# Optimization experiments

Hardware: AMD Instinct MI355X
Metric: run time of the kernel (lower is better)

## Reference

```python
import jax, jax.numpy as jnp
import numpy as np

B, S, D = 2, 2048, 512
H = 8
G = 4
LAMBDA_INIT = 0.2  # 0.8 - 0.6*exp(-0.3*(layer_idx-1)) with layer_idx=1
EPS = 1e-5


def setup_inputs() -> dict:
    key = jax.random.key(0)
    ks = jax.random.split(key, 16)
    n = jax.random.normal
    return {
        "x": n(ks[0], (B, S, D), jnp.float32),
        "K1_w": n(ks[1], (D, D), jnp.float32) * 0.02,
        "K1_b": n(ks[2], (D,), jnp.float32) * 0.02,
        "Q1_w": n(ks[3], (D, D), jnp.float32) * 0.02,
        "K2_w": n(ks[4], (D, D), jnp.float32) * 0.02,
        "K2_b": n(ks[5], (D,), jnp.float32) * 0.02,
        "Q2_w": n(ks[6], (D, D), jnp.float32) * 0.02,
        "V_w": n(ks[7], (D, D), jnp.float32) * 0.02,
        "lambda_q1": n(ks[8], (H, 1), jnp.float32),
        "lambda_k1": n(ks[9], (H, 1), jnp.float32),
        "lambda_q2": n(ks[10], (H, 1), jnp.float32),
        "lambda_k2": n(ks[11], (H, 1), jnp.float32),
        "gn_w": jnp.ones((D,), jnp.float32),
        "gn_b": jnp.zeros((D,), jnp.float32),
        "out_w": n(ks[12], (D, D), jnp.float32) * 0.02,
        "out_b": n(ks[13], (D,), jnp.float32) * 0.02,
    }


def reference(x, K1_w, K1_b, Q1_w, K2_w, K2_b, Q2_w, V_w,
              lambda_q1, lambda_k1, lambda_q2, lambda_k2,
              gn_w, gn_b, out_w, out_b):
    b, s, d = x.shape
    hd = d // H

    def heads(t):  # (b,s,d) -> (b,H,s,hd)
        return t.reshape(b, s, H, hd).transpose(0, 2, 1, 3)

    q1 = heads(x @ Q1_w.T)
    k1 = heads(x @ K1_w.T + K1_b)
    q2 = heads(x @ Q2_w.T)
    k2 = heads(x @ K2_w.T + K2_b)
    v = heads(x @ V_w.T)

    scale = hd ** 0.5
    a1 = jax.nn.softmax(jnp.einsum('bhqd,bhkd->bhqk', q1, k1) / scale, axis=-1)
    a2 = jax.nn.softmax(jnp.einsum('bhqd,bhkd->bhqk', q2, k2) / scale, axis=-1)

    lam = (jnp.exp(lambda_q1 * lambda_k1)
           - jnp.exp(lambda_q2 * lambda_k2) + LAMBDA_INIT)  # (H,1)
    attn = a1 - lam.reshape(1, H, 1, 1) * a2

    o = jnp.einsum('bhqk,bhkd->bhqd', attn, v)
    o = o.transpose(0, 2, 1, 3).reshape(b, s, d)

    # GroupNorm over channels: input (b, d, s), groups G normalize over (d/G, s)
    xc = o.transpose(0, 2, 1).reshape(b, G, d // G, s)
    mu = xc.mean(axis=(2, 3), keepdims=True)
    var = xc.var(axis=(2, 3), keepdims=True)
    xn = ((xc - mu) * jax.lax.rsqrt(var + EPS)).reshape(b, d, s)
    xn = xn * gn_w[None, :, None] + gn_b[None, :, None]

    y = xn.transpose(0, 2, 1) @ out_w.T + out_b
    return y
```

## Files before the change

### kernel.cpp

```cpp
#include <hip/hip_runtime.h>
#include <hip/hip_bf16.h>

typedef __bf16 bf16;
typedef __attribute__((ext_vector_type(4))) __bf16 bf16x4;
typedef __attribute__((ext_vector_type(8))) __bf16 bf16x8;
typedef __attribute__((ext_vector_type(4))) float f32x4;

#define MFMA16(a, b, c) __builtin_amdgcn_mfma_f32_16x16x32_bf16((a), (b), (c), 0, 0, 0)

static constexpr float EPS = 1e-5f;
static constexpr float LAMBDA_INIT = 0.2f;
static constexpr float LOG2E = 1.44269504088896340736f;

__device__ __forceinline__ bf16x8 cvt8(const float* p) {
    const f32x4 a = *(const f32x4*)p;
    const f32x4 b = *(const f32x4*)(p + 4);
    bf16x8 r;
    r[0] = (bf16)a[0]; r[1] = (bf16)a[1]; r[2] = (bf16)a[2]; r[3] = (bf16)a[3];
    r[4] = (bf16)b[0]; r[5] = (bf16)b[1]; r[6] = (bf16)b[2]; r[7] = (bf16)b[3];
    return r;
}

__device__ __forceinline__ void gload_lds16(const void* g, void* l) {
    __builtin_amdgcn_global_load_lds(
        (const __attribute__((address_space(1))) unsigned int*)g,
        (__attribute__((address_space(3))) unsigned int*)l,
        16, 0, 0);
}

__global__ __launch_bounds__(256) void prep_kernel(
    const float* __restrict__ x,
    const float* __restrict__ q1w, const float* __restrict__ k1w,
    const float* __restrict__ q2w, const float* __restrict__ k2w,
    const float* __restrict__ vw,
    const float* __restrict__ ow, const float* __restrict__ gnw,
    const float* __restrict__ gnb,
    bf16* __restrict__ xb, bf16* __restrict__ wb,
    bf16* __restrict__ owg, float* __restrict__ S0, float* __restrict__ stats)
{
    const int tid = threadIdx.x;
    if (blockIdx.x < 1664) {
        const size_t base = ((size_t)blockIdx.x * 256 + tid) * 8;
        if (base < 2097152) {
            *(bf16x8*)(xb + base) = cvt8(x + base);
        } else {
            const size_t wbase = base - 2097152;
            const int wsel = (int)(wbase >> 18);
            const size_t off = wbase & 262143;
            const float* W = (wsel == 0) ? q1w : (wsel == 1) ? k1w :
                             (wsel == 2) ? q2w : (wsel == 3) ? k2w : vw;
            *(bf16x8*)(wb + wbase) = cvt8(W + off);
        }
        return;
    }

    __shared__ float red[4];
    const int pb = blockIdx.x - 1664;
    if (pb == 0 && tid < 16) stats[tid] = 0.f;

    const int n0 = pb * 16;
    const int c0 = tid, c1 = tid + 256;
    const float gw0 = gnw[c0], gw1 = gnw[c1];
    const float gb0 = gnb[c0], gb1 = gnb[c1];

    for (int n = 0; n < 16; ++n) {
        const size_t rowb = (size_t)(n0 + n) * 512;
        const float w0 = ow[rowb + c0];
        const float w1 = ow[rowb + c1];
        owg[rowb + c0] = (bf16)(w0 * gw0);
        owg[rowb + c1] = (bf16)(w1 * gw1);
        float s = gb0 * w0 + gb1 * w1;
#pragma unroll
        for (int off = 1; off < 64; off <<= 1) s += __shfl_xor(s, off, 64);
        if ((tid & 63) == 0) red[tid >> 6] = s;
        __syncthreads();
        if (tid == 0) S0[n0 + n] = red[0] + red[1] + red[2] + red[3];
        __syncthreads();
    }
}

__global__ __launch_bounds__(256) void proj_kernel(
    const bf16* __restrict__ xb, const bf16* __restrict__ wb,
    const float* __restrict__ k1b, const float* __restrict__ k2b,
    bf16* __restrict__ q1o, bf16* __restrict__ k1o,
    bf16* __restrict__ q2o, bf16* __restrict__ k2o,
    bf16* __restrict__ vto)
{
    __shared__ __align__(16) bf16 sh[32768];
    bf16* const As0 = sh;
    bf16* const As1 = sh + 8192;
    bf16* const Bs0 = sh + 16384;
    bf16* const Bs1 = sh + 24576;

    const int tid = threadIdx.x;
    const int wave = tid >> 6, lane = tid & 63;
    const int l15 = lane & 15, quad = lane >> 4;
    const int wm = wave >> 1, wn = wave & 1;

    const int mb = blockIdx.x / 20;
    const int nb = blockIdx.x % 20;
    const int wsel = nb >> 2;
    const int nrow0 = (nb & 3) * 128;

    const int srow = lane >> 3;
    const int scol = 8 * ((lane & 7) ^ srow);
    const bf16* ag = xb + (size_t)(mb * 128 + srow) * 512 + scol;
    const bf16* bg = wb + (size_t)(wsel * 512 + nrow0 + srow) * 512 + scol;

    f32x4 acc[4][4];
#pragma unroll
    for (int i = 0; i < 4; ++i)
#pragma unroll
        for (int j = 0; j < 4; ++j)
            acc[i][j] = (f32x4){0.f, 0.f, 0.f, 0.f};

#define STAGE_PROJ(abuf, bbuf, s) do {                                         \
    const int k0_ = (s) * 64;                                                  \
    _Pragma("unroll")                                                          \
    for (int c_ = 0; c_ < 4; ++c_) {                                           \
        const int chunk_ = wave * 4 + c_;                                      \
        gload_lds16(ag + (size_t)(chunk_ * 8) * 512 + k0_, (abuf) + chunk_ * 512); \
        gload_lds16(bg + (size_t)(chunk_ * 8) * 512 + k0_, (bbuf) + chunk_ * 512); \
    }                                                                          \
} while (0)

    STAGE_PROJ(As0, Bs0, 0);
    __syncthreads();

    const int ka = 8 * (quad ^ (l15 & 7));

    for (int s = 0; s < 8; ++s) {
        const bf16* Ac = (s & 1) ? As1 : As0;
        const bf16* Bc = (s & 1) ? Bs1 : Bs0;
        if (s < 7) {
            if (s & 1) STAGE_PROJ(As0, Bs0, s + 1);
            else       STAGE_PROJ(As1, Bs1, s + 1);
        }

        bf16x8 al[4], ah[4], bl[4], bh_[4];
#pragma unroll
        for (int i = 0; i < 4; ++i) {
            const bf16* p = Ac + (wm * 64 + i * 16 + l15) * 64;
            al[i] = *(const bf16x8*)(p + ka);
            ah[i] = *(const bf16x8*)(p + (ka ^ 32));
        }
#pragma unroll
        for (int j = 0; j < 4; ++j) {
            const bf16* p = Bc + (wn * 64 + j * 16 + l15) * 64;
            bl[j]  = *(const bf16x8*)(p + ka);
            bh_[j] = *(const bf16x8*)(p + (ka ^ 32));
        }

#pragma unroll
        for (int i = 0; i < 4; ++i)
#pragma unroll
            for (int j = 0; j < 4; ++j) {
                acc[i][j] = MFMA16(al[i], bl[j], acc[i][j]);
                acc[i][j] = MFMA16(ah[i], bh_[j], acc[i][j]);
            }

        __syncthreads();
    }

    const int bidx = mb >> 4;
    const int sbase = (mb & 15) * 128;
    const float scale = (wsel == 0 || wsel == 2) ? 0.125f * LOG2E : 1.0f;

    if (wsel != 4) {
        bf16* const T = sh;
        const int swzq = quad << 4;
#pragma unroll
        for (int j = 0; j < 4; ++j) {
            const int nl = wn * 64 + j * 16 + l15;
            const int ncol = nrow0 + nl;
            float bias = 0.f;
            if (wsel == 1) bias = k1b[ncol];
            if (wsel == 3) bias = k2b[ncol];
            const int nswz = nl ^ swzq;
#pragma unroll
            for (int i = 0; i < 4; ++i) {
                const int mbase = wm * 64 + i * 16 + quad * 4;
#pragma unroll
                for (int r = 0; r < 4; ++r)
                    T[(mbase + r) * 128 + nswz] = (bf16)(acc[i][j][r] * scale + bias);
            }
        }
        __syncthreads();

        bf16* const dst = (wsel == 0) ? q1o : (wsel == 1) ? k1o :
                          (wsel == 2) ? q2o : k2o;
#pragma unroll
        for (int hsel = 0; hsel < 2; ++hsel) {
            const int h = (nrow0 >> 6) + hsel;
            bf16* db = dst + ((size_t)(bidx * 8 + h) * 2048 + sbase) * 64;
#pragma unroll
            for (int ps = 0; ps < 4; ++ps) {
                const int idx = (ps * 256 + tid) * 8;
                const int m = idx >> 6, hd = idx & 63;
                const bf16x8 v = *(const bf16x8*)(
                    T + m * 128 + ((hsel * 64 + hd) ^ (((m >> 2) & 3) << 4)));
                *(bf16x8*)(db + idx) = v;
            }
        }
    } else {
        bf16* const Tt = sh;
#pragma unroll
        for (int j = 0; j < 4; ++j) {
            const int nl = wn * 64 + j * 16 + l15;
            const int hd = (nrow0 + nl) & 63;
            const int xh = (hd >> 1) & 3;
            const int swz = (nl & 7) << 2;
#pragma unroll
            for (int i = 0; i < 4; ++i) {
                const int colb = (wm * 64 + (i >> 1) * 32 + ((quad ^ xh) << 3)
                                  + ((i & 1) << 2)) ^ swz;
                bf16x4 pk;
#pragma unroll
                for (int r = 0; r < 4; ++r) pk[r] = (bf16)acc[i][j][r];
                *(bf16x4*)(Tt + nl * 132 + colb) = pk;
            }
        }
        __syncthreads();

#pragma unroll
        for (int ps = 0; ps < 8; ++ps) {
            const int rown = ps * 16 + (tid >> 4);
            const int seg = tid & 15;
            const int swz = (rown & 7) << 2;
            const bf16x4 lo = *(const bf16x4*)(Tt + rown * 132 + ((seg * 8) ^ swz));
            const bf16x4 hi = *(const bf16x4*)(Tt + rown * 132 + ((seg * 8 + 4) ^ swz));
            const int ncol = nrow0 + rown;
            const int h = ncol >> 6, hd = ncol & 63;
            bf16x8 v;
            v[0] = lo[0]; v[1] = lo[1]; v[2] = lo[2]; v[3] = lo[3];
            v[4] = hi[0]; v[5] = hi[1]; v[6] = hi[2]; v[7] = hi[3];
            *(bf16x8*)(vto + ((size_t)(bidx * 8 + h) * 64 + hd) * 2048
                       + sbase + seg * 8) = v;
        }
    }
#undef STAGE_PROJ
}

__global__ __launch_bounds__(256, 2) void attn_kernel(
    const bf16* __restrict__ q1, const bf16* __restrict__ k1,
    const bf16* __restrict__ q2, const bf16* __restrict__ k2,
    const bf16* __restrict__ vt,
    const float* __restrict__ lq1, const float* __restrict__ lk1,
    const float* __restrict__ lq2, const float* __restrict__ lk2,
    bf16* __restrict__ o, float* __restrict__ stats)
{
    __shared__ __align__(16) bf16 smem[2][12288];
    __shared__ float lbuf[4][4][16];
    __shared__ float sred[2][2];

    const int tid = threadIdx.x;
    const int wave = tid >> 6;
    const int lane = tid & 63;
    const int l15 = lane & 15, quad = lane >> 4;
    const int qp = wave & 1;
    const int kg = wave >> 1;

    const int rid = (blockIdx.x & 7) * 64 + (blockIdx.x >> 3);
    const int bh = rid >> 5;
    const int qt = rid & 31;
    const int b = bh >> 3, h = bh & 7;

    const bf16* k1t = k1 + (size_t)bh * 2048 * 64;
    const bf16* k2t = k2 + (size_t)bh * 2048 * 64;
    const bf16* vtt = vt + (size_t)bh * 64 * 2048;

    const int qrow = qt * 64 + qp * 32 + l15;
    const bf16* q1p = q1 + ((size_t)bh * 2048 + qrow) * 64 + quad * 8;
    const bf16* q2p = q2 + ((size_t)bh * 2048 + qrow) * 64 + quad * 8;
    const bf16x8 q1A0 = *(const bf16x8*)(q1p);
    const bf16x8 q1A1 = *(const bf16x8*)(q1p + 32);
    const bf16x8 q1B0 = *(const bf16x8*)(q1p + 16 * 64);
    const bf16x8 q1B1 = *(const bf16x8*)(q1p + 16 * 64 + 32);
    const bf16x8 q2A0 = *(const bf16x8*)(q2p);
    const bf16x8 q2A1 = *(const bf16x8*)(q2p + 32);
    const bf16x8 q2B0 = *(const bf16x8*)(q2p + 16 * 64);
    const bf16x8 q2B1 = *(const bf16x8*)(q2p + 16 * 64 + 32);

    const int krow = lane >> 3;
    const int kcol = 8 * ((lane & 7) ^ krow);
    const int ko0 = (wave * 8 + krow) * 64 + kcol;
    const int ko1 = (1024 + wave * 8 + krow) * 64 + kcol;
    const int vrow = lane >> 2;
    const int vo0 = (wave * 16 + vrow) * 2048 + (lane & 3) * 8;
    const int vo1 = (wave * 16 + vrow) * 2048 + 1024 + (lane & 3) * 8;

#define STAGE_ATTN(buf, itv) do {                                   \
    const int ko_ = (itv) * 32 * 64;                                \
    const int vo_ = (itv) * 32;                                     \
    gload_lds16(k1t + ko0 + ko_, (buf) + wave * 512);               \
    gload_lds16(k1t + ko1 + ko_, (buf) + 2048 + wave * 512);        \
    gload_lds16(k2t + ko0 + ko_, (buf) + 4096 + wave * 512);        \
    gload_lds16(k2t + ko1 + ko_, (buf) + 6144 + wave * 512);        \
    gload_lds16(vtt + vo0 + vo_, (buf) + 8192 + wave * 512);        \
    gload_lds16(vtt + vo1 + vo_, (buf) + 10240 + wave * 512);       \
} while (0)

    const int koffa = 8 * (quad ^ (l15 & 7));
    const int koffb = 8 * ((quad + 4) ^ (l15 & 7));
    const int vsw = 8 * (quad ^ ((l15 >> 1) & 3));

    f32x4 O1A[4], O2A[4], O1B[4], O2B[4];
    float l1A = 0.f, l2A = 0.f, l1B = 0.f, l2B = 0.f;
#pragma unroll
    for (int t = 0; t < 4; ++t) {
        O1A[t] = (f32x4){0.f, 0.f, 0.f, 0.f};
        O2A[t] = (f32x4){0.f, 0.f, 0.f, 0.f};
        O1B[t] = (f32x4){0.f, 0.f, 0.f, 0.f};
        O2B[t] = (f32x4){0.f, 0.f, 0.f, 0.f};
    }

    STAGE_ATTN(smem[0], 0);
    __syncthreads();

    for (int it = 0; it < 32; ++it) {
        const bf16* sb = smem[it & 1];
        if (it < 31) STAGE_ATTN(smem[(it & 1) ^ 1], it + 1);

        const bf16* k1r = sb + kg * 2048;
        const bf16* k2r = sb + 4096 + kg * 2048;
        const bf16* vr  = sb + 8192 + kg * 2048;

        const bf16x8 k1t0a = *(const bf16x8*)(k1r + l15 * 64 + koffa);
        const bf16x8 k1t0b = *(const bf16x8*)(k1r + l15 * 64 + koffb);
        const bf16x8 k1t1a = *(const bf16x8*)(k1r + (16 + l15) * 64 + koffa);
        const bf16x8 k1t1b = *(const bf16x8*)(k1r + (16 + l15) * 64 + koffb);
        const bf16x8 k2t0a = *(const bf16x8*)(k2r + l15 * 64 + koffa);
        const bf16x8 k2t0b = *(const bf16x8*)(k2r + l15 * 64 + koffb);
        const bf16x8 k2t1a = *(const bf16x8*)(k2r + (16 + l15) * 64 + koffa);
        const bf16x8 k2t1b = *(const bf16x8*)(k2r + (16 + l15) * 64 + koffb);
        const bf16x8 v0 = *(const bf16x8*)(vr + l15 * 32 + vsw);
        const bf16x8 v1 = *(const bf16x8*)(vr + (16 + l15) * 32 + vsw);
        const bf16x8 v2 = *(const bf16x8*)(vr + (32 + l15) * 32 + vsw);
        const bf16x8 v3 = *(const bf16x8*)(vr + (48 + l15) * 32 + vsw);

        const f32x4 z = (f32x4){0.f, 0.f, 0.f, 0.f};
        __builtin_amdgcn_s_setprio(1);
        f32x4 s1t0A = MFMA16(k1t0a, q1A0, z);  s1t0A = MFMA16(k1t0b, q1A1, s1t0A);
        f32x4 s1t1A = MFMA16(k1t1a, q1A0, z);  s1t1A = MFMA16(k1t1b, q1A1, s1t1A);
        f32x4 s2t0A = MFMA16(k2t0a, q2A0, z);  s2t0A = MFMA16(k2t0b, q2A1, s2t0A);
        f32x4 s2t1A = MFMA16(k2t1a, q2A0, z);  s2t1A = MFMA16(k2t1b, q2A1, s2t1A);
        f32x4 s1t0B = MFMA16(k1t0a, q1B0, z);  s1t0B = MFMA16(k1t0b, q1B1, s1t0B);
        f32x4 s1t1B = MFMA16(k1t1a, q1B0, z);  s1t1B = MFMA16(k1t1b, q1B1, s1t1B);
        f32x4 s2t0B = MFMA16(k2t0a, q2B0, z);  s2t0B = MFMA16(k2t0b, q2B1, s2t0B);
        f32x4 s2t1B = MFMA16(k2t1a, q2B0, z);  s2t1B = MFMA16(k2t1b, q2B1, s2t1B);
        __builtin_amdgcn_s_setprio(0);

        bf16x8 b1A, b2A, b1B, b2B;
#pragma unroll
        for (int r = 0; r < 4; ++r) {
            float e;
            e = __builtin_amdgcn_exp2f(s1t0A[r]); l1A += e; b1A[r]     = (bf16)e;
            e = __builtin_amdgcn_exp2f(s1t1A[r]); l1A += e; b1A[4 + r] = (bf16)e;
            e = __builtin_amdgcn_exp2f(s2t0A[r]); l2A += e; b2A[r]     = (bf16)e;
            e = __builtin_amdgcn_exp2f(s2t1A[r]); l2A += e; b2A[4 + r] = (bf16)e;
            e = __builtin_amdgcn_exp2f(s1t0B[r]); l1B += e; b1B[r]     = (bf16)e;
            e = __builtin_amdgcn_exp2f(s1t1B[r]); l1B += e; b1B[4 + r] = (bf16)e;
            e = __builtin_amdgcn_exp2f(s2t0B[r]); l2B += e; b2B[r]     = (bf16)e;
            e = __builtin_amdgcn_exp2f(s2t1B[r]); l2B += e; b2B[4 + r] = (bf16)e;
        }

        __builtin_amdgcn_s_setprio(1);
        O1A[0] = MFMA16(v0, b1A, O1A[0]);  O1A[1] = MFMA16(v1, b1A, O1A[1]);
        O1A[2] = MFMA16(v2, b1A, O1A[2]);  O1A[3] = MFMA16(v3, b1A, O1A[3]);
        O2A[0] = MFMA16(v0, b2A, O2A[0]);  O2A[1] = MFMA16(v1, b2A, O2A[1]);
        O2A[2] = MFMA16(v2, b2A, O2A[2]);  O2A[3] = MFMA16(v3, b2A, O2A[3]);
        O1B[0] = MFMA16(v0, b1B, O1B[0]);  O1B[1] = MFMA16(v1, b1B, O1B[1]);
        O1B[2] = MFMA16(v2, b1B, O1B[2]);  O1B[3] = MFMA16(v3, b1B, O1B[3]);
        O2B[0] = MFMA16(v0, b2B, O2B[0]);  O2B[1] = MFMA16(v1, b2B, O2B[1]);
        O2B[2] = MFMA16(v2, b2B, O2B[2]);  O2B[3] = MFMA16(v3, b2B, O2B[3]);
        __builtin_amdgcn_s_setprio(0);

        __syncthreads();
    }

    l1A += __shfl_xor(l1A, 16, 64);  l1A += __shfl_xor(l1A, 32, 64);
    l2A += __shfl_xor(l2A, 16, 64);  l2A += __shfl_xor(l2A, 32, 64);
    l1B += __shfl_xor(l1B, 16, 64);  l1B += __shfl_xor(l1B, 32, 64);
    l2B += __shfl_xor(l2B, 16, 64);  l2B += __shfl_xor(l2B, 32, 64);
    if (lane < 16) {
        lbuf[wave][0][lane] = l1A;
        lbuf[wave][1][lane] = l2A;
        lbuf[wave][2][lane] = l1B;
        lbuf[wave][3][lane] = l2B;
    }

    f32x4* rb = (f32x4*)smem;
    if (kg == 1) {
        f32x4* dst = rb + qp * 1024;
#pragma unroll
        for (int t = 0; t < 4; ++t) {
            dst[t * 64 + lane]        = O1A[t];
            dst[(4 + t) * 64 + lane]  = O2A[t];
            dst[(8 + t) * 64 + lane]  = O1B[t];
            dst[(12 + t) * 64 + lane] = O2B[t];
        }
    }
    __syncthreads();

    float ssum = 0.f, ssq = 0.f;
    if (kg == 0) {
        const f32x4* src = rb + qp * 1024;
#pragma unroll
        for (int t = 0; t < 4; ++t) {
            O1A[t] += src[t * 64 + lane];
            O2A[t] += src[(4 + t) * 64 + lane];
            O1B[t] += src[(8 + t) * 64 + lane];
            O2B[t] += src[(12 + t) * 64 + lane];
        }
        const float L1A = l1A + lbuf[wave + 2][0][l15];
        const float L2A = l2A + lbuf[wave + 2][1][l15];
        const float L1B = l1B + lbuf[wave + 2][2][l15];
        const float L2B = l2B + lbuf[wave + 2][3][l15];
        const float lam = __expf(lq1[h] * lk1[h]) - __expf(lq2[h] * lk2[h]) + LAMBDA_INIT;
        const float i1A = 1.f / L1A, i2A = lam / L2A;
        const float i1B = 1.f / L1B, i2B = lam / L2B;
        const size_t rowA = (size_t)(b * 2048 + qt * 64 + qp * 32 + l15) * 512 + h * 64;
        const size_t rowB = rowA + 16 * 512;
#pragma unroll
        for (int t = 0; t < 4; ++t) {
#pragma unroll
            for (int r = 0; r < 4; ++r) {
                const float vA = O1A[t][r] * i1A - O2A[t][r] * i2A;
                const float vB = O1B[t][r] * i1B - O2B[t][r] * i2B;
                ssum += vA + vB;
                ssq += vA * vA + vB * vB;
                o[rowA + t * 16 + quad * 4 + r] = (bf16)vA;
                o[rowB + t * 16 + quad * 4 + r] = (bf16)vB;
            }
        }
    }
#pragma unroll
    for (int off = 1; off < 64; off <<= 1) {
        ssum += __shfl_xor(ssum, off, 64);
        ssq += __shfl_xor(ssq, off, 64);
    }
    if (kg == 0 && lane == 0) { sred[qp][0] = ssum; sred[qp][1] = ssq; }
    __syncthreads();
    if (tid == 0) {
        const float s0 = sred[0][0] + sred[1][0];
        const float s1 = sred[0][1] + sred[1][1];
        const int bg = b * 4 + (h >> 1);
        atomicAdd(&stats[bg * 2], s0);
        atomicAdd(&stats[bg * 2 + 1], s1);
    }
}

__global__ __launch_bounds__(256) void out_gemm_kernel(
    const bf16* __restrict__ o, const bf16* __restrict__ owg,
    const float* __restrict__ S0, const float* __restrict__ stats,
    const float* __restrict__ ob, float* __restrict__ y)
{
    __shared__ __align__(16) bf16 sh[16384];
    bf16* const As0 = sh;
    bf16* const As1 = sh + 4096;
    bf16* const Bs0 = sh + 8192;
    bf16* const Bs1 = sh + 12288;

    const int tid = threadIdx.x;
    const int wave = tid >> 6, lane = tid & 63;
    const int l15 = lane & 15, quad = lane >> 4;

    const int mb = blockIdx.x >> 3;
    const int nb = blockIdx.x & 7;
    const int b = mb >> 5;

    const float N = 128.f * 2048.f;
    float mu[4], rs[4];
#pragma unroll
    for (int g = 0; g < 4; ++g) {
        const float m = stats[(b * 4 + g) * 2] / N;
        const float var = stats[(b * 4 + g) * 2 + 1] / N - m * m;
        mu[g] = m;
        rs[g] = rsqrtf(var + EPS);
    }

    const int srow = lane >> 3;
    const int scol = 8 * ((lane & 7) ^ srow);
    const bf16* ag = o + (size_t)(mb * 64 + srow) * 512 + scol;
    const bf16* bg = owg + (size_t)(nb * 64 + srow) * 512 + scol;

#define STAGE_OUT(abuf, bbuf, s) do {                                          \
    const int k0_ = (s) * 64;                                                  \
    _Pragma("unroll")                                                          \
    for (int c_ = 0; c_ < 2; ++c_) {                                           \
        const int chunk_ = wave * 2 + c_;                                      \
        gload_lds16(ag + (size_t)(chunk_ * 8) * 512 + k0_, (abuf) + chunk_ * 512); \
        gload_lds16(bg + (size_t)(chunk_ * 8) * 512 + k0_, (bbuf) + chunk_ * 512); \
    }                                                                          \
} while (0)

    f32x4 acc[4], tot[4];
#pragma unroll
    for (int i = 0; i < 4; ++i) {
        acc[i] = (f32x4){0.f, 0.f, 0.f, 0.f};
        tot[i] = (f32x4){0.f, 0.f, 0.f, 0.f};
    }
    float s1g[4];
    float s1p = 0.f;
#pragma unroll
    for (int g = 0; g < 4; ++g) s1g[g] = 0.f;

    STAGE_OUT(As0, Bs0, 0);
    __syncthreads();

    const int ka = 8 * (quad ^ (l15 & 7));

    for (int kk = 0; kk < 8; ++kk) {
        const bf16* Ac = (kk & 1) ? As1 : As0;
        const bf16* Bc = (kk & 1) ? Bs1 : Bs0;
        if (kk < 7) {
            if (kk & 1) STAGE_OUT(As0, Bs0, kk + 1);
            else        STAGE_OUT(As1, Bs1, kk + 1);
        }

        bf16x8 al[4], ah[4];
#pragma unroll
        for (int i = 0; i < 4; ++i) {
            const bf16* p = Ac + (i * 16 + l15) * 64;
            al[i] = *(const bf16x8*)(p + ka);
            ah[i] = *(const bf16x8*)(p + (ka ^ 32));
        }
        const bf16* pb = Bc + (wave * 16 + l15) * 64;
        const bf16x8 bl = *(const bf16x8*)(pb + ka);
        const bf16x8 bh = *(const bf16x8*)(pb + (ka ^ 32));

#pragma unroll
        for (int i = 0; i < 4; ++i) {
            acc[i] = MFMA16(al[i], bl, acc[i]);
            acc[i] = MFMA16(ah[i], bh, acc[i]);
        }

#pragma unroll
        for (int j = 0; j < 8; ++j) s1p += (float)bl[j] + (float)bh[j];

        __syncthreads();

        if (kk & 1) {
            const int g = kk >> 1;
#pragma unroll
            for (int i = 0; i < 4; ++i) {
#pragma unroll
                for (int r = 0; r < 4; ++r) tot[i][r] += rs[g] * acc[i][r];
                acc[i] = (f32x4){0.f, 0.f, 0.f, 0.f};
            }
            float sg = s1p + __shfl_xor(s1p, 16, 64);
            sg += __shfl_xor(sg, 32, 64);
            s1g[g] = sg;
            s1p = 0.f;
        }
    }

    const int ncol = nb * 64 + wave * 16 + l15;
    float bias = S0[ncol] + ob[ncol];
#pragma unroll
    for (int g = 0; g < 4; ++g) bias -= mu[g] * rs[g] * s1g[g];

    float* const Tf = (float*)sh;
    const int nl = wave * 16 + l15;
#pragma unroll
    for (int i = 0; i < 4; ++i) {
        const int mbase = i * 16 + quad * 4;
#pragma unroll
        for (int r = 0; r < 4; ++r)
            Tf[(mbase + r) * 64 + (nl ^ (quad << 4))] = tot[i][r] + bias;
    }
    __syncthreads();

#pragma unroll
    for (int ps = 0; ps < 4; ++ps) {
        const int idx = (ps * 256 + tid) * 4;
        const int m = idx >> 6, n4 = idx & 63;
        const f32x4 v = *(const f32x4*)(Tf + m * 64 + (n4 ^ (((m >> 2) & 3) << 4)));
        *(f32x4*)(y + (size_t)(mb * 64 + m) * 512 + nb * 64 + n4) = v;
    }
#undef STAGE_OUT
}

extern "C" void kernel_launch(void* const* d_in, const int* in_sizes, int n_in,
                              void* d_out, int out_size, void* d_ws, size_t ws_size,
                              hipStream_t stream)
{
    const float* x   = (const float*)d_in[0];
    const float* K1w = (const float*)d_in[1];
    const float* K1b = (const float*)d_in[2];
    const float* Q1w = (const float*)d_in[3];
    const float* K2w = (const float*)d_in[4];
    const float* K2b = (const float*)d_in[5];
    const float* Q2w = (const float*)d_in[6];
    const float* Vw  = (const float*)d_in[7];
    const float* lq1 = (const float*)d_in[8];
    const float* lk1 = (const float*)d_in[9];
    const float* lq2 = (const float*)d_in[10];
    const float* lk2 = (const float*)d_in[11];
    const float* gnw = (const float*)d_in[12];
    const float* gnb = (const float*)d_in[13];
    const float* Ow  = (const float*)d_in[14];
    const float* Ob  = (const float*)d_in[15];

    const size_t SZ = (size_t)2 * 8 * 2048 * 64;
    bf16* q1 = (bf16*)d_ws;
    bf16* k1 = q1 + SZ;
    bf16* q2 = k1 + SZ;
    bf16* k2 = q2 + SZ;
    bf16* vt = k2 + SZ;
    bf16* o  = vt + SZ;
    bf16* xb = o;
    bf16* wb = o + SZ;
    bf16* owg = wb + (size_t)2560 * 512;
    float* S0 = (float*)(owg + 512 * 512);
    float* stats = S0 + 512;

    prep_kernel<<<1696, 256, 0, stream>>>(x, Q1w, K1w, Q2w, K2w, Vw,
                                          Ow, gnw, gnb, xb, wb, owg, S0, stats);
    proj_kernel<<<640, 256, 0, stream>>>(xb, wb, K1b, K2b,
                                         q1, k1, q2, k2, vt);
    attn_kernel<<<512, 256, 0, stream>>>(q1, k1, q2, k2, vt,
                                         lq1, lk1, lq2, lk2, o, stats);
    out_gemm_kernel<<<512, 256, 0, stream>>>(o, owg, S0, stats, Ob,
                                             (float*)d_out);
}
```

Baseline: 176.8 us.

## Use 8-wave attention blocks with triple-buffered LDS and raw waitcnt barriers

The attention kernel goes from 4 to 8 waves per block. Each wave now owns one 16-row query tile instead of two, and the final two-stage cross-wave reduction of O is restructured to match. Both the attention kernel and the output GEMM switch from double to triple buffering, prefetching two stages ahead and syncing with s_waitcnt vmcnt plus s_barrier instead of two __syncthreads per iteration. The aim is better latency hiding and more waves in flight. The cost is more LDS per block, which may limit occupancy, and a more fragile reliance on exact vmcnt counts.

Measured after the change: 174.6 us. Within noise of the previous version (-1.2%).

```diff
diff --git a/kernel.cpp b/kernel.cpp
--- a/kernel.cpp
+++ b/kernel.cpp
@@ -241,7 +241,7 @@
 #undef STAGE_PROJ
 }
 
-__global__ __launch_bounds__(256, 2) void attn_kernel(
+__global__ __launch_bounds__(512, 4) void attn_kernel(
     const bf16* __restrict__ q1, const bf16* __restrict__ k1,
     const bf16* __restrict__ q2, const bf16* __restrict__ k2,
     const bf16* __restrict__ vt,
@@ -249,16 +249,16 @@
     const float* __restrict__ lq2, const float* __restrict__ lk2,
     bf16* __restrict__ o, float* __restrict__ stats)
 {
-    __shared__ __align__(16) bf16 smem[2][12288];
-    __shared__ float lbuf[4][4][16];
-    __shared__ float sred[2][2];
+    __shared__ __align__(16) bf16 smem[3][12288];
+    __shared__ float lbuf[8][2][16];
+    __shared__ float sred[8][2];
 
     const int tid = threadIdx.x;
     const int wave = tid >> 6;
     const int lane = tid & 63;
     const int l15 = lane & 15, quad = lane >> 4;
-    const int qp = wave & 1;
-    const int kg = wave >> 1;
+    const int qtile = wave & 3;
+    const int kg = wave >> 2;
 
     const int rid = (blockIdx.x & 7) * 64 + (blockIdx.x >> 3);
     const int bh = rid >> 5;
@@ -269,57 +269,54 @@
     const bf16* k2t = k2 + (size_t)bh * 2048 * 64;
     const bf16* vtt = vt + (size_t)bh * 64 * 2048;
 
-    const int qrow = qt * 64 + qp * 32 + l15;
+    const int qrow = qt * 64 + qtile * 16 + l15;
     const bf16* q1p = q1 + ((size_t)bh * 2048 + qrow) * 64 + quad * 8;
     const bf16* q2p = q2 + ((size_t)bh * 2048 + qrow) * 64 + quad * 8;
-    const bf16x8 q1A0 = *(const bf16x8*)(q1p);
-    const bf16x8 q1A1 = *(const bf16x8*)(q1p + 32);
-    const bf16x8 q1B0 = *(const bf16x8*)(q1p + 16 * 64);
-    const bf16x8 q1B1 = *(const bf16x8*)(q1p + 16 * 64 + 32);
-    const bf16x8 q2A0 = *(const bf16x8*)(q2p);
-    const bf16x8 q2A1 = *(const bf16x8*)(q2p + 32);
-    const bf16x8 q2B0 = *(const bf16x8*)(q2p + 16 * 64);
-    const bf16x8 q2B1 = *(const bf16x8*)(q2p + 16 * 64 + 32);
-
-    const int krow = lane >> 3;
-    const int kcol = 8 * ((lane & 7) ^ krow);
-    const int ko0 = (wave * 8 + krow) * 64 + kcol;
-    const int ko1 = (1024 + wave * 8 + krow) * 64 + kcol;
-    const int vrow = lane >> 2;
-    const int vo0 = (wave * 16 + vrow) * 2048 + (lane & 3) * 8;
-    const int vo1 = (wave * 16 + vrow) * 2048 + 1024 + (lane & 3) * 8;
+    const bf16x8 q1f0 = *(const bf16x8*)(q1p);
+    const bf16x8 q1f1 = *(const bf16x8*)(q1p + 32);
+    const bf16x8 q2f0 = *(const bf16x8*)(q2p);
+    const bf16x8 q2f1 = *(const bf16x8*)(q2p + 32);
+
+    const int sw = wave & 3;
+    const int skey0 = (wave < 4) ? 0 : 1024;
+    const size_t ksrc0 = (size_t)(skey0 + sw * 8 + (lane >> 3)) * 64
+                       + 8 * ((lane & 7) ^ (lane >> 3));
+    const size_t vsrc0 = (size_t)(sw * 16 + (lane >> 2)) * 2048 + skey0 + (lane & 3) * 8;
 
 #define STAGE_ATTN(buf, itv) do {                                   \
-    const int ko_ = (itv) * 32 * 64;                                \
-    const int vo_ = (itv) * 32;                                     \
-    gload_lds16(k1t + ko0 + ko_, (buf) + wave * 512);               \
-    gload_lds16(k1t + ko1 + ko_, (buf) + 2048 + wave * 512);        \
-    gload_lds16(k2t + ko0 + ko_, (buf) + 4096 + wave * 512);        \
-    gload_lds16(k2t + ko1 + ko_, (buf) + 6144 + wave * 512);        \
-    gload_lds16(vtt + vo0 + vo_, (buf) + 8192 + wave * 512);        \
-    gload_lds16(vtt + vo1 + vo_, (buf) + 10240 + wave * 512);       \
+    const size_t koff_ = ksrc0 + (size_t)(itv) * 32 * 64;           \
+    gload_lds16(k1t + koff_, (buf) + wave * 512);                   \
+    gload_lds16(k2t + koff_, (buf) + 4096 + wave * 512);            \
+    gload_lds16(vtt + vsrc0 + (itv) * 32, (buf) + 8192 + wave * 512); \
 } while (0)
 
     const int koffa = 8 * (quad ^ (l15 & 7));
     const int koffb = 8 * ((quad + 4) ^ (l15 & 7));
     const int vsw = 8 * (quad ^ ((l15 >> 1) & 3));
 
-    f32x4 O1A[4], O2A[4], O1B[4], O2B[4];
-    float l1A = 0.f, l2A = 0.f, l1B = 0.f, l2B = 0.f;
+    f32x4 O1[4], O2[4];
+    float l1 = 0.f, l2 = 0.f;
 #pragma unroll
     for (int t = 0; t < 4; ++t) {
-        O1A[t] = (f32x4){0.f, 0.f, 0.f, 0.f};
-        O2A[t] = (f32x4){0.f, 0.f, 0.f, 0.f};
-        O1B[t] = (f32x4){0.f, 0.f, 0.f, 0.f};
-        O2B[t] = (f32x4){0.f, 0.f, 0.f, 0.f};
+        O1[t] = (f32x4){0.f, 0.f, 0.f, 0.f};
+        O2[t] = (f32x4){0.f, 0.f, 0.f, 0.f};
     }
 
     STAGE_ATTN(smem[0], 0);
-    __syncthreads();
-
+    STAGE_ATTN(smem[1], 1);
+
+    int cur = 0;
     for (int it = 0; it < 32; ++it) {
-        const bf16* sb = smem[it & 1];
-        if (it < 31) STAGE_ATTN(smem[(it & 1) ^ 1], it + 1);
+        if (it < 31) {
+            asm volatile("s_waitcnt vmcnt(3)\ns_barrier" ::: "memory");
+        } else {
+            asm volatile("s_waitcnt vmcnt(0)\ns_barrier" ::: "memory");
+        }
+        __builtin_amdgcn_sched_barrier(0);
+
+        const bf16* sb = smem[cur];
+        const int n2 = (cur == 0) ? 2 : cur - 1;
+        if (it < 30) STAGE_ATTN(smem[n2], it + 2);
 
         const bf16* k1r = sb + kg * 2048;
         const bf16* k2r = sb + 4096 + kg * 2048;
@@ -340,97 +337,97 @@
 
         const f32x4 z = (f32x4){0.f, 0.f, 0.f, 0.f};
         __builtin_amdgcn_s_setprio(1);
-        f32x4 s1t0A = MFMA16(k1t0a, q1A0, z);  s1t0A = MFMA16(k1t0b, q1A1, s1t0A);
-        f32x4 s1t1A = MFMA16(k1t1a, q1A0, z);  s1t1A = MFMA16(k1t1b, q1A1, s1t1A);
-        f32x4 s2t0A = MFMA16(k2t0a, q2A0, z);  s2t0A = MFMA16(k2t0b, q2A1, s2t0A);
-        f32x4 s2t1A = MFMA16(k2t1a, q2A0, z);  s2t1A = MFMA16(k2t1b, q2A1, s2t1A);
-        f32x4 s1t0B = MFMA16(k1t0a, q1B0, z);  s1t0B = MFMA16(k1t0b, q1B1, s1t0B);
-        f32x4 s1t1B = MFMA16(k1t1a, q1B0, z);  s1t1B = MFMA16(k1t1b, q1B1, s1t1B);
-        f32x4 s2t0B = MFMA16(k2t0a, q2B0, z);  s2t0B = MFMA16(k2t0b, q2B1, s2t0B);
-        f32x4 s2t1B = MFMA16(k2t1a, q2B0, z);  s2t1B = MFMA16(k2t1b, q2B1, s2t1B);
+        f32x4 s1t0 = MFMA16(k1t0a, q1f0, z);  s1t0 = MFMA16(k1t0b, q1f1, s1t0);
+        f32x4 s1t1 = MFMA16(k1t1a, q1f0, z);  s1t1 = MFMA16(k1t1b, q1f1, s1t1);
+        f32x4 s2t0 = MFMA16(k2t0a, q2f0, z);  s2t0 = MFMA16(k2t0b, q2f1, s2t0);
+        f32x4 s2t1 = MFMA16(k2t1a, q2f0, z);  s2t1 = MFMA16(k2t1b, q2f1, s2t1);
         __builtin_amdgcn_s_setprio(0);
 
-        bf16x8 b1A, b2A, b1B, b2B;
+        bf16x8 b1, b2;
 #pragma unroll
         for (int r = 0; r < 4; ++r) {
             float e;
-            e = __builtin_amdgcn_exp2f(s1t0A[r]); l1A += e; b1A[r]     = (bf16)e;
-            e = __builtin_amdgcn_exp2f(s1t1A[r]); l1A += e; b1A[4 + r] = (bf16)e;
-            e = __builtin_amdgcn_exp2f(s2t0A[r]); l2A += e; b2A[r]     = (bf16)e;
-            e = __builtin_amdgcn_exp2f(s2t1A[r]); l2A += e; b2A[4 + r] = (bf16)e;
-            e = __builtin_amdgcn_exp2f(s1t0B[r]); l1B += e; b1B[r]     = (bf16)e;
-            e = __builtin_amdgcn_exp2f(s1t1B[r]); l1B += e; b1B[4 + r] = (bf16)e;
-            e = __builtin_amdgcn_exp2f(s2t0B[r]); l2B += e; b2B[r]     = (bf16)e;
-            e = __builtin_amdgcn_exp2f(s2t1B[r]); l2B += e; b2B[4 + r] = (bf16)e;
+            e = __builtin_amdgcn_exp2f(s1t0[r]); l1 += e; b1[r]     = (bf16)e;
+            e = __builtin_amdgcn_exp2f(s1t1[r]); l1 += e; b1[4 + r] = (bf16)e;
+            e = __builtin_amdgcn_exp2f(s2t0[r]); l2 += e; b2[r]     = (bf16)e;
+            e = __builtin_amdgcn_exp2f(s2t1[r]); l2 += e; b2[4 + r] = (bf16)e;
         }
 
         __builtin_amdgcn_s_setprio(1);
-        O1A[0] = MFMA16(v0, b1A, O1A[0]);  O1A[1] = MFMA16(v1, b1A, O1A[1]);
-        O1A[2] = MFMA16(v2, b1A, O1A[2]);  O1A[3] = MFMA16(v3, b1A, O1A[3]);
-        O2A[0] = MFMA16(v0, b2A, O2A[0]);  O2A[1] = MFMA16(v1, b2A, O2A[1]);
-        O2A[2] = MFMA16(v2, b2A, O2A[2]);  O2A[3] = MFMA16(v3, b2A, O2A[3]);
-        O1B[0] = MFMA16(v0, b1B, O1B[0]);  O1B[1] = MFMA16(v1, b1B, O1B[1]);
-        O1B[2] = MFMA16(v2, b1B, O1B[2]);  O1B[3] = MFMA16(v3, b1B, O1B[3]);
-        O2B[0] = MFMA16(v0, b2B, O2B[0]);  O2B[1] = MFMA16(v1, b2B, O2B[1]);
-        O2B[2] = MFMA16(v2, b2B, O2B[2]);  O2B[3] = MFMA16(v3, b2B, O2B[3]);
+        O1[0] = MFMA16(v0, b1, O1[0]);
+        O1[1] = MFMA16(v1, b1, O1[1]);
+        O1[2] = MFMA16(v2, b1, O1[2]);
+        O1[3] = MFMA16(v3, b1, O1[3]);
+        O2[0] = MFMA16(v0, b2, O2[0]);
+        O2[1] = MFMA16(v1, b2, O2[1]);
+        O2[2] = MFMA16(v2, b2, O2[2]);
+        O2[3] = MFMA16(v3, b2, O2[3]);
         __builtin_amdgcn_s_setprio(0);
 
-        __syncthreads();
-    }
-
-    l1A += __shfl_xor(l1A, 16, 64);  l1A += __shfl_xor(l1A, 32, 64);
-    l2A += __shfl_xor(l2A, 16, 64);  l2A += __shfl_xor(l2A, 32, 64);
-    l1B += __shfl_xor(l1B, 16, 64);  l1B += __shfl_xor(l1B, 32, 64);
-    l2B += __shfl_xor(l2B, 16, 64);  l2B += __shfl_xor(l2B, 32, 64);
+        cur = (cur == 2) ? 0 : cur + 1;
+    }
+
+    l1 += __shfl_xor(l1, 16, 64);  l1 += __shfl_xor(l1, 32, 64);
+    l2 += __shfl_xor(l2, 16, 64);  l2 += __shfl_xor(l2, 32, 64);
     if (lane < 16) {
-        lbuf[wave][0][lane] = l1A;
-        lbuf[wave][1][lane] = l2A;
-        lbuf[wave][2][lane] = l1B;
-        lbuf[wave][3][lane] = l2B;
-    }
+        lbuf[wave][0][lane] = l1;
+        lbuf[wave][1][lane] = l2;
+    }
+    __syncthreads();
 
     f32x4* rb = (f32x4*)smem;
-    if (kg == 1) {
-        f32x4* dst = rb + qp * 1024;
+    if (wave == 4 || wave == 5) {
+        f32x4* dst = rb + (wave - 4) * 512;
 #pragma unroll
         for (int t = 0; t < 4; ++t) {
-            dst[t * 64 + lane]        = O1A[t];
-            dst[(4 + t) * 64 + lane]  = O2A[t];
-            dst[(8 + t) * 64 + lane]  = O1B[t];
-            dst[(12 + t) * 64 + lane] = O2B[t];
-        }
-    }
-    __syncthreads();
+            dst[t * 64 + lane]       = O1[t];
+            dst[(4 + t) * 64 + lane] = O2[t];
+        }
+    }
+    __syncthreads();
+    if (wave == 0 || wave == 1) {
+        const f32x4* src = rb + wave * 512;
+#pragma unroll
+        for (int t = 0; t < 4; ++t) {
+            O1[t] += src[t * 64 + lane];
+            O2[t] += src[(4 + t) * 64 + lane];
+        }
+    }
+    __syncthreads();
+    if (wave == 6 || wave == 7) {
+        f32x4* dst = rb + (wave - 6) * 512;
+#pragma unroll
+        for (int t = 0; t < 4; ++t) {
+            dst[t * 64 + lane]       = O1[t];
+            dst[(4 + t) * 64 + lane] = O2[t];
+        }
+    }
+    __syncthreads();
+    if (wave == 2 || wave == 3) {
+        const f32x4* src = rb + (wave - 2) * 512;
+#pragma unroll
+        for (int t = 0; t < 4; ++t) {
+            O1[t] += src[t * 64 + lane];
+            O2[t] += src[(4 + t) * 64 + lane];
+        }
+    }
 
     float ssum = 0.f, ssq = 0.f;
-    if (kg == 0) {
-        const f32x4* src = rb + qp * 1024;
+    if (wave < 4) {
+        const float L1 = l1 + lbuf[wave + 4][0][l15];
+        const float L2 = l2 + lbuf[wave + 4][1][l15];
+        const float lam = __expf(lq1[h] * lk1[h]) - __expf(lq2[h] * lk2[h]) + LAMBDA_INIT;
+        const float inv1 = 1.f / L1;
+        const float inv2 = lam / L2;
+        const size_t row = (size_t)(b * 2048 + qt * 64 + wave * 16 + l15) * 512 + h * 64;
 #pragma unroll
         for (int t = 0; t < 4; ++t) {
-            O1A[t] += src[t * 64 + lane];
-            O2A[t] += src[(4 + t) * 64 + lane];
-            O1B[t] += src[(8 + t) * 64 + lane];
-            O2B[t] += src[(12 + t) * 64 + lane];
-        }
-        const float L1A = l1A + lbuf[wave + 2][0][l15];
-        const float L2A = l2A + lbuf[wave + 2][1][l15];
-        const float L1B = l1B + lbuf[wave + 2][2][l15];
-        const float L2B = l2B + lbuf[wave + 2][3][l15];
-        const float lam = __expf(lq1[h] * lk1[h]) - __expf(lq2[h] * lk2[h]) + LAMBDA_INIT;
-        const float i1A = 1.f / L1A, i2A = lam / L2A;
-        const float i1B = 1.f / L1B, i2B = lam / L2B;
-        const size_t rowA = (size_t)(b * 2048 + qt * 64 + qp * 32 + l15) * 512 + h * 64;
-        const size_t rowB = rowA + 16 * 512;
-#pragma unroll
-        for (int t = 0; t < 4; ++t) {
 #pragma unroll
             for (int r = 0; r < 4; ++r) {
-                const float vA = O1A[t][r] * i1A - O2A[t][r] * i2A;
-                const float vB = O1B[t][r] * i1B - O2B[t][r] * i2B;
-                ssum += vA + vB;
-                ssq += vA * vA + vB * vB;
-                o[rowA + t * 16 + quad * 4 + r] = (bf16)vA;
-                o[rowB + t * 16 + quad * 4 + r] = (bf16)vB;
+                const float val = O1[t][r] * inv1 - O2[t][r] * inv2;
+                ssum += val;
+                ssq += val * val;
+                o[row + t * 16 + quad * 4 + r] = (bf16)val;
             }
         }
     }
@@ -439,15 +436,16 @@
         ssum += __shfl_xor(ssum, off, 64);
         ssq += __shfl_xor(ssq, off, 64);
     }
-    if (kg == 0 && lane == 0) { sred[qp][0] = ssum; sred[qp][1] = ssq; }
+    if (lane == 0) { sred[wave][0] = ssum; sred[wave][1] = ssq; }
     __syncthreads();
     if (tid == 0) {
-        const float s0 = sred[0][0] + sred[1][0];
-        const float s1 = sred[0][1] + sred[1][1];
+        float s0 = 0.f, s1 = 0.f;
+        for (int w = 0; w < 8; ++w) { s0 += sred[w][0]; s1 += sred[w][1]; }
         const int bg = b * 4 + (h >> 1);
         atomicAdd(&stats[bg * 2], s0);
         atomicAdd(&stats[bg * 2 + 1], s1);
     }
+#undef STAGE_ATTN
 }
 
 __global__ __launch_bounds__(256) void out_gemm_kernel(
@@ -455,11 +453,7 @@
     const float* __restrict__ S0, const float* __restrict__ stats,
     const float* __restrict__ ob, float* __restrict__ y)
 {
-    __shared__ __align__(16) bf16 sh[16384];
-    bf16* const As0 = sh;
-    bf16* const As1 = sh + 4096;
-    bf16* const Bs0 = sh + 8192;
-    bf16* const Bs1 = sh + 12288;
+    __shared__ __align__(16) bf16 sh[24576];
 
     const int tid = threadIdx.x;
     const int wave = tid >> 6, lane = tid & 63;
@@ -505,18 +499,24 @@
 #pragma unroll
     for (int g = 0; g < 4; ++g) s1g[g] = 0.f;
 
-    STAGE_OUT(As0, Bs0, 0);
-    __syncthreads();
+    STAGE_OUT(sh, sh + 12288, 0);
+    STAGE_OUT(sh + 4096, sh + 12288 + 4096, 1);
 
     const int ka = 8 * (quad ^ (l15 & 7));
 
+    int cur = 0;
     for (int kk = 0; kk < 8; ++kk) {
-        const bf16* Ac = (kk & 1) ? As1 : As0;
-        const bf16* Bc = (kk & 1) ? Bs1 : Bs0;
         if (kk < 7) {
-            if (kk & 1) STAGE_OUT(As0, Bs0, kk + 1);
-            else        STAGE_OUT(As1, Bs1, kk + 1);
-        }
+            asm volatile("s_waitcnt vmcnt(4)\ns_barrier" ::: "memory");
+        } else {
+            asm volatile("s_waitcnt vmcnt(0)\ns_barrier" ::: "memory");
+        }
+        __builtin_amdgcn_sched_barrier(0);
+
+        const bf16* Ac = sh + cur * 4096;
+        const bf16* Bc = sh + 12288 + cur * 4096;
+        const int n2 = (cur == 0) ? 2 : cur - 1;
+        if (kk < 6) STAGE_OUT(sh + n2 * 4096, sh + 12288 + n2 * 4096, kk + 2);
 
         bf16x8 al[4], ah[4];
 #pragma unroll
@@ -537,8 +537,6 @@
 
 #pragma unroll
         for (int j = 0; j < 8; ++j) s1p += (float)bl[j] + (float)bh[j];
-
-        __syncthreads();
 
         if (kk & 1) {
             const int g = kk >> 1;
@@ -553,7 +551,10 @@
             s1g[g] = sg;
             s1p = 0.f;
         }
-    }
+
+        cur = (cur == 2) ? 0 : cur + 1;
+    }
+    __syncthreads();
 
     const int ncol = nb * 64 + wave * 16 + l15;
     float bias = S0[ncol] + ob[ncol];
@@ -619,7 +620,7 @@
                                           Ow, gnw, gnb, xb, wb, owg, S0, stats);
     proj_kernel<<<640, 256, 0, stream>>>(xb, wb, K1b, K2b,
                                          q1, k1, q2, k2, vt);
-    attn_kernel<<<512, 256, 0, stream>>>(q1, k1, q2, k2, vt,
+    attn_kernel<<<512, 512, 0, stream>>>(q1, k1, q2, k2, vt,
                                          lq1, lk1, lq2, lk2, o, stats);
     out_gemm_kernel<<<512, 256, 0, stream>>>(o, owg, S0, stats, Ob,
                                              (float*)d_out);
```
